# Kernel tuning notes

Measured on AMD Instinct MI355X. Metric: run time of the kernel, lower is better.

## Reference

```python
import jax, jax.numpy as jnp
import numpy as np

N_NODES = 50000
N_EDGES = 800000
F_DIM = 64
NEG_SLOPE_ATT = 0.2   # GATConv attention LeakyReLU
NEG_SLOPE_ACT = 0.01  # nn.LeakyReLU default between layers


def setup_inputs() -> dict:
    key = jax.random.key(0)
    ks = jax.random.split(key, 10)
    s = 1.0 / np.sqrt(F_DIM)
    return {
        "x": jax.random.normal(ks[0], (N_NODES, F_DIM), jnp.float32),
        "edge_index": jax.random.randint(ks[1], (2, N_EDGES), 0, N_NODES, jnp.int64),
        "W0": jax.random.normal(ks[2], (F_DIM, F_DIM), jnp.float32) * s,
        "a_src0": jax.random.normal(ks[3], (F_DIM,), jnp.float32) * s,
        "a_dst0": jax.random.normal(ks[4], (F_DIM,), jnp.float32) * s,
        "b0": jnp.zeros((F_DIM,), jnp.float32),
        "W1": jax.random.normal(ks[5], (F_DIM, F_DIM), jnp.float32) * s,
        "a_src1": jax.random.normal(ks[6], (F_DIM,), jnp.float32) * s,
        "a_dst1": jax.random.normal(ks[7], (F_DIM,), jnp.float32) * s,
        "b1": jnp.zeros((F_DIM,), jnp.float32),
    }


def _gat_layer(x, src, dst, W, a_src, a_dst, b, n_nodes):
    # x: [N,F]; src/dst: [E'] (self-loops included)
    h = x @ W                                   # [N,F]
    alpha_s = h @ a_src                          # [N]
    alpha_d = h @ a_dst                          # [N]
    e = jax.nn.leaky_relu(alpha_s[src] + alpha_d[dst], NEG_SLOPE_ATT)  # [E']
    # scatter-softmax over incoming edges per destination node
    m = jax.ops.segment_max(e, dst, num_segments=n_nodes)              # [N]
    ex = jnp.exp(e - m[dst])                                           # [E']
    z = jax.ops.segment_sum(ex, dst, num_segments=n_nodes)             # [N]
    alpha = ex / (z[dst] + 1e-16)                                      # [E']
    out = jax.ops.segment_sum(h[src] * alpha[:, None], dst, num_segments=n_nodes)
    return out + b


def reference(x, edge_index, W0, a_src0, a_dst0, b0, W1, a_src1, a_dst1, b1):
    n = x.shape[0]
    loops = jnp.arange(n, dtype=edge_index.dtype)
    src = jnp.concatenate([edge_index[0], loops])  # add_self_loops=True
    dst = jnp.concatenate([edge_index[1], loops])
    h = _gat_layer(x, src, dst, W0, a_src0, a_dst0, b0, n)
    h = jax.nn.leaky_relu(h, NEG_SLOPE_ACT)
    h = _gat_layer(h, src, dst, W1, a_src1, a_dst1, b1, n)
    h = jax.nn.leaky_relu(h, NEG_SLOPE_ACT)
    return h + x  # residual with original input features
```

## Files before the change

kernel.cpp:

```cpp
#include <hip/hip_runtime.h>
#include <math.h>

#define NNODES 50000
#define NEDGES 800000
#define ETOT   850000
#define F      64
#define NB     782
#define CAP    1408
#define LIN_BLOCKS 3125
#define AGG_BLOCKS 1563
#define SBLK   256
#define SIT    13
#define SEPB   (256 * SIT)

typedef unsigned short u16;
typedef unsigned int   u32;

__device__ __forceinline__ u32 f2bf2(float a, float b) {
    u32 ua = __float_as_uint(a), ub = __float_as_uint(b);
    ua = (ua + 0x7FFFu + ((ua >> 16) & 1u)) >> 16;
    ub = (ub + 0x7FFFu + ((ub >> 16) & 1u)) >> 16;
    return ua | (ub << 16);
}

struct LinSmem {
    float Ws[F * F];
    float xs[16][F + 1];
    float asv[F], adv[F];
};

__device__ __forceinline__ void linear_body(
    LinSmem& sm,
    const float* __restrict__ x, const float* __restrict__ W,
    const float* __restrict__ a_src, const float* __restrict__ a_dst,
    u16* __restrict__ h16, float* __restrict__ as_, float* __restrict__ ad_,
    int blk)
{
    const int tid = threadIdx.x;
    const int wv  = tid >> 6;
    const int ln  = tid & 63;
    const int q   = ln >> 4;
    const int fl4 = (ln & 15) * 4;
    const int nb  = wv * 4 + q;
    const int node = blk * 16 + nb;

    for (int i = tid * 4; i < F * F; i += 1024)
        *(float4*)&sm.Ws[i] = *(const float4*)&W[i];
    if (tid < F) { sm.asv[tid] = a_src[tid]; sm.adv[tid] = a_dst[tid]; }
    {
        const int n  = tid >> 4;
        const int c4 = (tid & 15) * 4;
        const float4 v = *(const float4*)&x[(size_t)(blk * 16 + n) * F + c4];
        sm.xs[n][c4] = v.x; sm.xs[n][c4+1] = v.y;
        sm.xs[n][c4+2] = v.z; sm.xs[n][c4+3] = v.w;
    }
    __syncthreads();

    float4 acc = {0.f, 0.f, 0.f, 0.f};
#pragma unroll
    for (int k = 0; k < F; ++k) {
        const float xv = sm.xs[nb][k];
        const float4 w = *(const float4*)&sm.Ws[k * F + fl4];
        acc.x = fmaf(xv, w.x, acc.x);
        acc.y = fmaf(xv, w.y, acc.y);
        acc.z = fmaf(xv, w.z, acc.z);
        acc.w = fmaf(xv, w.w, acc.w);
    }

    uint2 p;
    p.x = f2bf2(acc.x, acc.y);
    p.y = f2bf2(acc.z, acc.w);
    *(uint2*)(h16 + (size_t)node * F + fl4) = p;

    float vs = acc.x * sm.asv[fl4] + acc.y * sm.asv[fl4+1]
             + acc.z * sm.asv[fl4+2] + acc.w * sm.asv[fl4+3];
    float vd = acc.x * sm.adv[fl4] + acc.y * sm.adv[fl4+1]
             + acc.z * sm.adv[fl4+2] + acc.w * sm.adv[fl4+3];
#pragma unroll
    for (int off = 1; off < 16; off <<= 1) {
        vs += __shfl_xor(vs, off, 64);
        vd += __shfl_xor(vd, off, 64);
    }
    if ((ln & 15) == 0) { as_[node] = vs; ad_[node] = vd; }
}

__global__ __launch_bounds__(256) void stage_linear1(
    const float* __restrict__ x, const float* __restrict__ W,
    const float* __restrict__ a_src, const float* __restrict__ a_dst,
    u16* __restrict__ h16, float* __restrict__ as_, float* __restrict__ ad_,
    const int* __restrict__ src, const int* __restrict__ dst,
    int* __restrict__ gcur, u32* __restrict__ stg)
{
    __shared__ LinSmem sm;
    if (blockIdx.x < SBLK) {
        int* cnt  = (int*)&sm;
        int* lcur = cnt + NB;
        for (int i = threadIdx.x; i < NB; i += 256) cnt[i] = 0;
        __syncthreads();
        const int base = blockIdx.x * SEPB;
#pragma unroll
        for (int it = 0; it < SIT; ++it) {
            const int e = base + it * 256 + threadIdx.x;
            if (e < ETOT) {
                const int d = (e < NEDGES) ? dst[e] : (e - NEDGES);
                atomicAdd(&cnt[d >> 6], 1);
            }
        }
        __syncthreads();
        for (int i = threadIdx.x; i < NB; i += 256)
            lcur[i] = cnt[i] ? (i * CAP + atomicAdd(&gcur[i], cnt[i])) : 0;
        __syncthreads();
#pragma unroll
        for (int it = 0; it < SIT; ++it) {
            const int e = base + it * 256 + threadIdx.x;
            if (e < ETOT) {
                int s, d;
                if (e < NEDGES) { s = src[e]; d = dst[e]; }
                else            { s = e - NEDGES; d = s; }
                const int p = atomicAdd(&lcur[d >> 6], 1);
                stg[p] = ((u32)(d & 63) << 16) | (u32)s;
            }
        }
        return;
    }
    linear_body(sm, x, W, a_src, a_dst, h16, as_, ad_, blockIdx.x - SBLK);
}

__global__ __launch_bounds__(256) void bucket_csr(
    const int* __restrict__ gcur, const u32* __restrict__ stg,
    u16* __restrict__ csr, int* __restrict__ rowptr, int* __restrict__ rowcnt)
{
    __shared__ int cnt[64];
    const int b = blockIdx.x;
    const int nbase = b << 6;
    const int nr  = (NNODES - nbase < 64) ? (NNODES - nbase) : 64;
    const int beg = b * CAP;
    const int m   = gcur[b];

    if (threadIdx.x < 64) cnt[threadIdx.x] = 0;
    __syncthreads();
    for (int i = threadIdx.x; i < m; i += 256)
        atomicAdd(&cnt[stg[beg + i] >> 16], 1);
    __syncthreads();
    if (threadIdx.x < 64) {
        const int v = cnt[threadIdx.x];
        int incl = v;
#pragma unroll
        for (int off = 1; off < 64; off <<= 1) {
            const int t = __shfl_up(incl, off, 64);
            if (threadIdx.x >= off) incl += t;
        }
        const int pos = beg + incl - v;
        cnt[threadIdx.x] = pos;
        if (threadIdx.x < nr) {
            rowptr[nbase + threadIdx.x] = pos;
            rowcnt[nbase + threadIdx.x] = v;
        }
    }
    __syncthreads();
    for (int i = threadIdx.x; i < m; i += 256) {
        const u32 pk = stg[beg + i];
        const int pos = atomicAdd(&cnt[pk >> 16], 1);
        csr[pos] = (u16)(pk & 0xFFFFu);
    }
}

#define XSP 68
template<int MODE>
__global__ __launch_bounds__(256) void gat_agg(
    const int* __restrict__ rowptr, const int* __restrict__ rowcnt,
    const u16* __restrict__ csr, const u16* __restrict__ hin,
    const float* __restrict__ as_, const float* __restrict__ ad_,
    const float* __restrict__ bias,
    const float* __restrict__ Wn, const float* __restrict__ an_s,
    const float* __restrict__ an_d,
    u16* __restrict__ hout, float* __restrict__ as_out, float* __restrict__ ad_out,
    const float* __restrict__ resid, float* __restrict__ out)
{
    __shared__ float Ws[MODE == 0 ? F * F : 1];
    __shared__ float asv[MODE == 0 ? F : 1], adv[MODE == 0 ? F : 1];
    __shared__ float xs[MODE == 0 ? 32 * XSP : 1];

    const int tid = threadIdx.x;
    const int ln  = tid & 63;
    const int g   = ln >> 3;
    const int l   = ln & 7;
    const int nb  = (tid >> 6) * 8 + g;
    const int node = blockIdx.x * 32 + nb;
    const bool valid = node < NNODES;

    if constexpr (MODE == 0) {
        for (int i = tid * 4; i < F * F; i += 1024)
            *(float4*)&Ws[i] = *(const float4*)&Wn[i];
        if (tid < F) { asv[tid] = an_s[tid]; adv[tid] = an_d[tid]; }
    }

    int beg = 0, cnt = 0;
    float ad_n = 0.f;
    if (valid) {
        beg  = rowptr[node];
        cnt  = rowcnt[node];
        ad_n = ad_[node];
    }

    float a0=0.f,a1=0.f,a2=0.f,a3=0.f,a4=0.f,a5=0.f,a6=0.f,a7=0.f;
    float z = 0.f;
    int i = 0;
    for (; i + 1 < cnt; i += 2) {
        const int s1 = csr[beg + i];
        const int s2 = csr[beg + i + 1];
        const float r1 = as_[s1] + ad_n;
        const float r2 = as_[s2] + ad_n;
        const uint4 h1 = ((const uint4*)(hin + (size_t)s1 * F))[l];
        const uint4 h2 = ((const uint4*)(hin + (size_t)s2 * F))[l];
        const float t1 = (r1 > 0.f) ? r1 : 0.2f * r1;
        const float t2 = (r2 > 0.f) ? r2 : 0.2f * r2;
        const float e1 = __expf(t1);
        const float e2 = __expf(t2);
        z += e1 + e2;
        a0 = fmaf(e1, __uint_as_float(h1.x << 16),         a0);
        a1 = fmaf(e1, __uint_as_float(h1.x & 0xFFFF0000u), a1);
        a2 = fmaf(e1, __uint_as_float(h1.y << 16),         a2);
        a3 = fmaf(e1, __uint_as_float(h1.y & 0xFFFF0000u), a3);
        a4 = fmaf(e1, __uint_as_float(h1.z << 16),         a4);
        a5 = fmaf(e1, __uint_as_float(h1.z & 0xFFFF0000u), a5);
        a6 = fmaf(e1, __uint_as_float(h1.w << 16),         a6);
        a7 = fmaf(e1, __uint_as_float(h1.w & 0xFFFF0000u), a7);
        a0 = fmaf(e2, __uint_as_float(h2.x << 16),         a0);
        a1 = fmaf(e2, __uint_as_float(h2.x & 0xFFFF0000u), a1);
        a2 = fmaf(e2, __uint_as_float(h2.y << 16),         a2);
        a3 = fmaf(e2, __uint_as_float(h2.y & 0xFFFF0000u), a3);
        a4 = fmaf(e2, __uint_as_float(h2.z << 16),         a4);
        a5 = fmaf(e2, __uint_as_float(h2.z & 0xFFFF0000u), a5);
        a6 = fmaf(e2, __uint_as_float(h2.w << 16),         a6);
        a7 = fmaf(e2, __uint_as_float(h2.w & 0xFFFF0000u), a7);
    }
    if (i < cnt) {
        const int s1 = csr[beg + i];
        const float r1 = as_[s1] + ad_n;
        const uint4 h1 = ((const uint4*)(hin + (size_t)s1 * F))[l];
        const float t1 = (r1 > 0.f) ? r1 : 0.2f * r1;
        const float e1 = __expf(t1);
        z += e1;
        a0 = fmaf(e1, __uint_as_float(h1.x << 16),         a0);
        a1 = fmaf(e1, __uint_as_float(h1.x & 0xFFFF0000u), a1);
        a2 = fmaf(e1, __uint_as_float(h1.y << 16),         a2);
        a3 = fmaf(e1, __uint_as_float(h1.y & 0xFFFF0000u), a3);
        a4 = fmaf(e1, __uint_as_float(h1.z << 16),         a4);
        a5 = fmaf(e1, __uint_as_float(h1.z & 0xFFFF0000u), a5);
        a6 = fmaf(e1, __uint_as_float(h1.w << 16),         a6);
        a7 = fmaf(e1, __uint_as_float(h1.w & 0xFFFF0000u), a7);
    }

    const float inv = 1.f / (z + 1e-16f);
    const float4 b0v = *(const float4*)&bias[l * 8];
    const float4 b1v = *(const float4*)&bias[l * 8 + 4];
    float v0 = a0 * inv + b0v.x, v1 = a1 * inv + b0v.y;
    float v2 = a2 * inv + b0v.z, v3 = a3 * inv + b0v.w;
    float v4 = a4 * inv + b1v.x, v5 = a5 * inv + b1v.y;
    float v6 = a6 * inv + b1v.z, v7 = a7 * inv + b1v.w;
    v0 = (v0 > 0.f) ? v0 : 0.01f * v0;  v1 = (v1 > 0.f) ? v1 : 0.01f * v1;
    v2 = (v2 > 0.f) ? v2 : 0.01f * v2;  v3 = (v3 > 0.f) ? v3 : 0.01f * v3;
    v4 = (v4 > 0.f) ? v4 : 0.01f * v4;  v5 = (v5 > 0.f) ? v5 : 0.01f * v5;
    v6 = (v6 > 0.f) ? v6 : 0.01f * v6;  v7 = (v7 > 0.f) ? v7 : 0.01f * v7;

    if constexpr (MODE == 0) {
        {
            float4 w0; w0.x = v0; w0.y = v1; w0.z = v2; w0.w = v3;
            float4 w1; w1.x = v4; w1.y = v5; w1.z = v6; w1.w = v7;
            const int xb = nb * XSP + l * 8;
            *(float4*)&xs[xb]     = w0;
            *(float4*)&xs[xb + 4] = w1;
        }
        __syncthreads();

        const int nb2 = tid >> 3;
        const int c0  = (tid & 7) * 8;
        float o0=0.f,o1=0.f,o2=0.f,o3=0.f,o4=0.f,o5=0.f,o6=0.f,o7=0.f;
#pragma unroll 8
        for (int k = 0; k < F; ++k) {
            const float xv = xs[nb2 * XSP + k];
            const float4 wa = *(const float4*)&Ws[k * F + c0];
            const float4 wb = *(const float4*)&Ws[k * F + c0 + 4];
            o0 = fmaf(xv, wa.x, o0); o1 = fmaf(xv, wa.y, o1);
            o2 = fmaf(xv, wa.z, o2); o3 = fmaf(xv, wa.w, o3);
            o4 = fmaf(xv, wb.x, o4); o5 = fmaf(xv, wb.y, o5);
            o6 = fmaf(xv, wb.z, o6); o7 = fmaf(xv, wb.w, o7);
        }
        const int node2 = blockIdx.x * 32 + nb2;
        float vs = o0*asv[c0]   + o1*asv[c0+1] + o2*asv[c0+2] + o3*asv[c0+3]
                 + o4*asv[c0+4] + o5*asv[c0+5] + o6*asv[c0+6] + o7*asv[c0+7];
        float vd = o0*adv[c0]   + o1*adv[c0+1] + o2*adv[c0+2] + o3*adv[c0+3]
                 + o4*adv[c0+4] + o5*adv[c0+5] + o6*adv[c0+6] + o7*adv[c0+7];
        vs += __shfl_xor(vs, 1, 64); vs += __shfl_xor(vs, 2, 64); vs += __shfl_xor(vs, 4, 64);
        vd += __shfl_xor(vd, 1, 64); vd += __shfl_xor(vd, 2, 64); vd += __shfl_xor(vd, 4, 64);
        if (node2 < NNODES) {
            if ((tid & 7) == 0) { as_out[node2] = vs; ad_out[node2] = vd; }
            uint4 p;
            p.x = f2bf2(o0, o1); p.y = f2bf2(o2, o3);
            p.z = f2bf2(o4, o5); p.w = f2bf2(o6, o7);
            *(uint4*)&hout[(size_t)node2 * F + c0] = p;
        }
    } else {
        if (valid) {
            const float4 r0 = *(const float4*)(resid + (size_t)node * F + l * 8);
            const float4 r1 = *(const float4*)(resid + (size_t)node * F + l * 8 + 4);
            float4 o0, o1;
            o0.x = v0 + r0.x; o0.y = v1 + r0.y; o0.z = v2 + r0.z; o0.w = v3 + r0.w;
            o1.x = v4 + r1.x; o1.y = v5 + r1.y; o1.z = v6 + r1.z; o1.w = v7 + r1.w;
            *(float4*)(out + (size_t)node * F + l * 8)     = o0;
            *(float4*)(out + (size_t)node * F + l * 8 + 4) = o1;
        }
    }
}

extern "C" void kernel_launch(void* const* d_in, const int* in_sizes, int n_in,
                              void* d_out, int out_size, void* d_ws, size_t ws_size,
                              hipStream_t stream)
{
    const float* x   = (const float*)d_in[0];
    const int*   ei  = (const int*)  d_in[1];
    const float* W0  = (const float*)d_in[2];
    const float* as0 = (const float*)d_in[3];
    const float* ad0 = (const float*)d_in[4];
    const float* b0  = (const float*)d_in[5];
    const float* W1  = (const float*)d_in[6];
    const float* as1 = (const float*)d_in[7];
    const float* ad1 = (const float*)d_in[8];
    const float* b1  = (const float*)d_in[9];
    float* out = (float*)d_out;

    const int* src = ei;
    const int* dst = ei + NEDGES;

    char* ws = (char*)d_ws;
    u16*   h16    = (u16*)ws;   ws += (size_t)NNODES * F * 2;
    u16*   h2_16  = (u16*)ws;   ws += (size_t)NNODES * F * 2;
    float* as_    = (float*)ws; ws += (size_t)NNODES * 4;
    float* ad_    = (float*)ws; ws += (size_t)NNODES * 4;
    float* as2    = (float*)ws; ws += (size_t)NNODES * 4;
    float* ad2    = (float*)ws; ws += (size_t)NNODES * 4;
    int*   rowptr = (int*)ws;   ws += (size_t)NNODES * 4;
    int*   rowcnt = (int*)ws;   ws += (size_t)NNODES * 4;
    int*   gcur   = (int*)ws;   ws += (size_t)NB * 4;
    u32*   stg    = (u32*)ws;   ws += (size_t)NB * CAP * 4;
    u16*   csr    = (u16*)ws;   ws += (size_t)NB * CAP * 2;

    hipMemsetAsync(gcur, 0, (size_t)NB * 4, stream);
    stage_linear1<<<SBLK + LIN_BLOCKS, 256, 0, stream>>>(
        x, W0, as0, ad0, h16, as_, ad_, src, dst, gcur, stg);
    bucket_csr<<<NB, 256, 0, stream>>>(gcur, stg, csr, rowptr, rowcnt);

    gat_agg<0><<<AGG_BLOCKS, 256, 0, stream>>>(
        rowptr, rowcnt, csr, h16, as_, ad_, b0,
        W1, as1, ad1, h2_16, as2, ad2, nullptr, nullptr);
    gat_agg<1><<<AGG_BLOCKS, 256, 0, stream>>>(
        rowptr, rowcnt, csr, h2_16, as2, ad2, b1,
        nullptr, nullptr, nullptr, nullptr, nullptr, nullptr, x, out);
}
```

Before: 171.7 us.

## Widen linear tile to 32 nodes, cache edges in registers, unroll aggregation by four

The first-layer linear is remapped so each thread computes 8 outputs for one of 32 nodes per block, halving LIN_BLOCKS and using wider bf16 stores with bounds checks. The edge-bucketing prologue now keeps src/dst in registers between the count pass and the scatter pass, so edges are read from global memory once instead of twice. The GAT aggregation loop is unrolled to four edges per iteration with a predicated tail, so more independent gathers are in flight. The costs are higher register pressure, which may lower occupancy, and a redundant gather for padded tail edges.

After: 170.4 us. No clear change (-0.8%).

```diff
diff --git a/kernel.cpp b/kernel.cpp
--- a/kernel.cpp
+++ b/kernel.cpp
@@ -7,11 +7,12 @@
 #define F      64
 #define NB     782
 #define CAP    1408
-#define LIN_BLOCKS 3125
+#define LIN_BLOCKS 1563
 #define AGG_BLOCKS 1563
 #define SBLK   256
 #define SIT    13
 #define SEPB   (256 * SIT)
+#define XSP    68
 
 typedef unsigned short u16;
 typedef unsigned int   u32;
@@ -23,9 +24,19 @@
     return ua | (ub << 16);
 }
 
+#define ACC8(ev, hv) \
+    a0 = fmaf(ev, __uint_as_float(hv.x << 16),         a0); \
+    a1 = fmaf(ev, __uint_as_float(hv.x & 0xFFFF0000u), a1); \
+    a2 = fmaf(ev, __uint_as_float(hv.y << 16),         a2); \
+    a3 = fmaf(ev, __uint_as_float(hv.y & 0xFFFF0000u), a3); \
+    a4 = fmaf(ev, __uint_as_float(hv.z << 16),         a4); \
+    a5 = fmaf(ev, __uint_as_float(hv.z & 0xFFFF0000u), a5); \
+    a6 = fmaf(ev, __uint_as_float(hv.w << 16),         a6); \
+    a7 = fmaf(ev, __uint_as_float(hv.w & 0xFFFF0000u), a7)
+
 struct LinSmem {
     float Ws[F * F];
-    float xs[16][F + 1];
+    float xs[32 * XSP];
     float asv[F], adv[F];
 };
 
@@ -37,51 +48,48 @@
     int blk)
 {
     const int tid = threadIdx.x;
-    const int wv  = tid >> 6;
-    const int ln  = tid & 63;
-    const int q   = ln >> 4;
-    const int fl4 = (ln & 15) * 4;
-    const int nb  = wv * 4 + q;
-    const int node = blk * 16 + nb;
+    const int n   = tid >> 3;
+    const int c0  = (tid & 7) * 8;
+    const int node = blk * 32 + n;
+    const bool valid = node < NNODES;
 
     for (int i = tid * 4; i < F * F; i += 1024)
         *(float4*)&sm.Ws[i] = *(const float4*)&W[i];
     if (tid < F) { sm.asv[tid] = a_src[tid]; sm.adv[tid] = a_dst[tid]; }
-    {
-        const int n  = tid >> 4;
-        const int c4 = (tid & 15) * 4;
-        const float4 v = *(const float4*)&x[(size_t)(blk * 16 + n) * F + c4];
-        sm.xs[n][c4] = v.x; sm.xs[n][c4+1] = v.y;
-        sm.xs[n][c4+2] = v.z; sm.xs[n][c4+3] = v.w;
+    if (valid) {
+        const float4 v0 = *(const float4*)&x[(size_t)node * F + c0];
+        const float4 v1 = *(const float4*)&x[(size_t)node * F + c0 + 4];
+        *(float4*)&sm.xs[n * XSP + c0]     = v0;
+        *(float4*)&sm.xs[n * XSP + c0 + 4] = v1;
     }
     __syncthreads();
 
-    float4 acc = {0.f, 0.f, 0.f, 0.f};
-#pragma unroll
+    float o0=0.f,o1=0.f,o2=0.f,o3=0.f,o4=0.f,o5=0.f,o6=0.f,o7=0.f;
+#pragma unroll 8
     for (int k = 0; k < F; ++k) {
-        const float xv = sm.xs[nb][k];
-        const float4 w = *(const float4*)&sm.Ws[k * F + fl4];
-        acc.x = fmaf(xv, w.x, acc.x);
-        acc.y = fmaf(xv, w.y, acc.y);
-        acc.z = fmaf(xv, w.z, acc.z);
-        acc.w = fmaf(xv, w.w, acc.w);
-    }
-
-    uint2 p;
-    p.x = f2bf2(acc.x, acc.y);
-    p.y = f2bf2(acc.z, acc.w);
-    *(uint2*)(h16 + (size_t)node * F + fl4) = p;
-
-    float vs = acc.x * sm.asv[fl4] + acc.y * sm.asv[fl4+1]
-             + acc.z * sm.asv[fl4+2] + acc.w * sm.asv[fl4+3];
-    float vd = acc.x * sm.adv[fl4] + acc.y * sm.adv[fl4+1]
-             + acc.z * sm.adv[fl4+2] + acc.w * sm.adv[fl4+3];
-#pragma unroll
-    for (int off = 1; off < 16; off <<= 1) {
-        vs += __shfl_xor(vs, off, 64);
-        vd += __shfl_xor(vd, off, 64);
-    }
-    if ((ln & 15) == 0) { as_[node] = vs; ad_[node] = vd; }
+        const float xv = sm.xs[n * XSP + k];
+        const float4 wa = *(const float4*)&sm.Ws[k * F + c0];
+        const float4 wb = *(const float4*)&sm.Ws[k * F + c0 + 4];
+        o0 = fmaf(xv, wa.x, o0); o1 = fmaf(xv, wa.y, o1);
+        o2 = fmaf(xv, wa.z, o2); o3 = fmaf(xv, wa.w, o3);
+        o4 = fmaf(xv, wb.x, o4); o5 = fmaf(xv, wb.y, o5);
+        o6 = fmaf(xv, wb.z, o6); o7 = fmaf(xv, wb.w, o7);
+    }
+
+    float vs = o0*sm.asv[c0]   + o1*sm.asv[c0+1] + o2*sm.asv[c0+2] + o3*sm.asv[c0+3]
+             + o4*sm.asv[c0+4] + o5*sm.asv[c0+5] + o6*sm.asv[c0+6] + o7*sm.asv[c0+7];
+    float vd = o0*sm.adv[c0]   + o1*sm.adv[c0+1] + o2*sm.adv[c0+2] + o3*sm.adv[c0+3]
+             + o4*sm.adv[c0+4] + o5*sm.adv[c0+5] + o6*sm.adv[c0+6] + o7*sm.adv[c0+7];
+    vs += __shfl_xor(vs, 1, 64); vs += __shfl_xor(vs, 2, 64); vs += __shfl_xor(vs, 4, 64);
+    vd += __shfl_xor(vd, 1, 64); vd += __shfl_xor(vd, 2, 64); vd += __shfl_xor(vd, 4, 64);
+
+    if (valid) {
+        if ((tid & 7) == 0) { as_[node] = vs; ad_[node] = vd; }
+        uint4 p;
+        p.x = f2bf2(o0, o1); p.y = f2bf2(o2, o3);
+        p.z = f2bf2(o4, o5); p.w = f2bf2(o6, o7);
+        *(uint4*)&h16[(size_t)node * F + c0] = p;
+    }
 }
 
 __global__ __launch_bounds__(256) void stage_linear1(
@@ -98,18 +106,7 @@
         for (int i = threadIdx.x; i < NB; i += 256) cnt[i] = 0;
         __syncthreads();
         const int base = blockIdx.x * SEPB;
-#pragma unroll
-        for (int it = 0; it < SIT; ++it) {
-            const int e = base + it * 256 + threadIdx.x;
-            if (e < ETOT) {
-                const int d = (e < NEDGES) ? dst[e] : (e - NEDGES);
-                atomicAdd(&cnt[d >> 6], 1);
-            }
-        }
-        __syncthreads();
-        for (int i = threadIdx.x; i < NB; i += 256)
-            lcur[i] = cnt[i] ? (i * CAP + atomicAdd(&gcur[i], cnt[i])) : 0;
-        __syncthreads();
+        int es[SIT], ed[SIT];
 #pragma unroll
         for (int it = 0; it < SIT; ++it) {
             const int e = base + it * 256 + threadIdx.x;
@@ -117,8 +114,21 @@
                 int s, d;
                 if (e < NEDGES) { s = src[e]; d = dst[e]; }
                 else            { s = e - NEDGES; d = s; }
-                const int p = atomicAdd(&lcur[d >> 6], 1);
-                stg[p] = ((u32)(d & 63) << 16) | (u32)s;
+                es[it] = s; ed[it] = d;
+                atomicAdd(&cnt[d >> 6], 1);
+            } else {
+                ed[it] = -1; es[it] = 0;
+            }
+        }
+        __syncthreads();
+        for (int i = threadIdx.x; i < NB; i += 256)
+            lcur[i] = cnt[i] ? (i * CAP + atomicAdd(&gcur[i], cnt[i])) : 0;
+        __syncthreads();
+#pragma unroll
+        for (int it = 0; it < SIT; ++it) {
+            if (ed[it] >= 0) {
+                const int p = atomicAdd(&lcur[ed[it] >> 6], 1);
+                stg[p] = ((u32)(ed[it] & 63) << 16) | (u32)es[it];
             }
         }
         return;
@@ -165,7 +175,6 @@
     }
 }
 
-#define XSP 68
 template<int MODE>
 __global__ __launch_bounds__(256) void gat_agg(
     const int* __restrict__ rowptr, const int* __restrict__ rowcnt,
@@ -205,51 +214,52 @@
 
     float a0=0.f,a1=0.f,a2=0.f,a3=0.f,a4=0.f,a5=0.f,a6=0.f,a7=0.f;
     float z = 0.f;
+    const int nfull = cnt & ~3;
     int i = 0;
-    for (; i + 1 < cnt; i += 2) {
+    for (; i < nfull; i += 4) {
         const int s1 = csr[beg + i];
         const int s2 = csr[beg + i + 1];
+        const int s3 = csr[beg + i + 2];
+        const int s4 = csr[beg + i + 3];
         const float r1 = as_[s1] + ad_n;
         const float r2 = as_[s2] + ad_n;
+        const float r3 = as_[s3] + ad_n;
+        const float r4 = as_[s4] + ad_n;
         const uint4 h1 = ((const uint4*)(hin + (size_t)s1 * F))[l];
         const uint4 h2 = ((const uint4*)(hin + (size_t)s2 * F))[l];
+        const uint4 h3 = ((const uint4*)(hin + (size_t)s3 * F))[l];
+        const uint4 h4 = ((const uint4*)(hin + (size_t)s4 * F))[l];
         const float t1 = (r1 > 0.f) ? r1 : 0.2f * r1;
         const float t2 = (r2 > 0.f) ? r2 : 0.2f * r2;
+        const float t3 = (r3 > 0.f) ? r3 : 0.2f * r3;
+        const float t4 = (r4 > 0.f) ? r4 : 0.2f * r4;
         const float e1 = __expf(t1);
         const float e2 = __expf(t2);
-        z += e1 + e2;
-        a0 = fmaf(e1, __uint_as_float(h1.x << 16),         a0);
-        a1 = fmaf(e1, __uint_as_float(h1.x & 0xFFFF0000u), a1);
-        a2 = fmaf(e1, __uint_as_float(h1.y << 16),         a2);
-        a3 = fmaf(e1, __uint_as_float(h1.y & 0xFFFF0000u), a3);
-        a4 = fmaf(e1, __uint_as_float(h1.z << 16),         a4);
-        a5 = fmaf(e1, __uint_as_float(h1.z & 0xFFFF0000u), a5);
-        a6 = fmaf(e1, __uint_as_float(h1.w << 16),         a6);
-        a7 = fmaf(e1, __uint_as_float(h1.w & 0xFFFF0000u), a7);
-        a0 = fmaf(e2, __uint_as_float(h2.x << 16),         a0);
-        a1 = fmaf(e2, __uint_as_float(h2.x & 0xFFFF0000u), a1);
-        a2 = fmaf(e2, __uint_as_float(h2.y << 16),         a2);
-        a3 = fmaf(e2, __uint_as_float(h2.y & 0xFFFF0000u), a3);
-        a4 = fmaf(e2, __uint_as_float(h2.z << 16),         a4);
-        a5 = fmaf(e2, __uint_as_float(h2.z & 0xFFFF0000u), a5);
-        a6 = fmaf(e2, __uint_as_float(h2.w << 16),         a6);
-        a7 = fmaf(e2, __uint_as_float(h2.w & 0xFFFF0000u), a7);
+        const float e3 = __expf(t3);
+        const float e4 = __expf(t4);
+        z += (e1 + e2) + (e3 + e4);
+        ACC8(e1, h1); ACC8(e2, h2); ACC8(e3, h3); ACC8(e4, h4);
     }
     if (i < cnt) {
+        const int j2 = (i + 1 < cnt) ? (i + 1) : i;
+        const int j3 = (i + 2 < cnt) ? (i + 2) : i;
         const int s1 = csr[beg + i];
+        const int s2 = csr[beg + j2];
+        const int s3 = csr[beg + j3];
         const float r1 = as_[s1] + ad_n;
+        const float r2 = as_[s2] + ad_n;
+        const float r3 = as_[s3] + ad_n;
         const uint4 h1 = ((const uint4*)(hin + (size_t)s1 * F))[l];
+        const uint4 h2 = ((const uint4*)(hin + (size_t)s2 * F))[l];
+        const uint4 h3 = ((const uint4*)(hin + (size_t)s3 * F))[l];
         const float t1 = (r1 > 0.f) ? r1 : 0.2f * r1;
+        const float t2 = (r2 > 0.f) ? r2 : 0.2f * r2;
+        const float t3 = (r3 > 0.f) ? r3 : 0.2f * r3;
         const float e1 = __expf(t1);
-        z += e1;
-        a0 = fmaf(e1, __uint_as_float(h1.x << 16),         a0);
-        a1 = fmaf(e1, __uint_as_float(h1.x & 0xFFFF0000u), a1);
-        a2 = fmaf(e1, __uint_as_float(h1.y << 16),         a2);
-        a3 = fmaf(e1, __uint_as_float(h1.y & 0xFFFF0000u), a3);
-        a4 = fmaf(e1, __uint_as_float(h1.z << 16),         a4);
-        a5 = fmaf(e1, __uint_as_float(h1.z & 0xFFFF0000u), a5);
-        a6 = fmaf(e1, __uint_as_float(h1.w << 16),         a6);
-        a7 = fmaf(e1, __uint_as_float(h1.w & 0xFFFF0000u), a7);
+        const float e2 = (i + 1 < cnt) ? __expf(t2) : 0.f;
+        const float e3 = (i + 2 < cnt) ? __expf(t3) : 0.f;
+        z += e1 + e2 + e3;
+        ACC8(e1, h1); ACC8(e2, h2); ACC8(e3, h3);
     }
 
     const float inv = 1.f / (z + 1e-16f);
```
